# Kernel tuning notes

Measured on AMD Instinct MI355X. Metric: run time of the kernel, lower is better.

Reference implementation:

```python
import jax, jax.numpy as jnp
import numpy as np

EPS = 1e-6

def _sobel_grad_mag(x):
    # x: [B, C, H, W]. Kernels are cross-correlation (as F.conv2d):
    # vertical:   out[i,j] = -x[i-1,j] + x[i+1,j]
    # horizontal: out[i,j] = -x[i,j-1] + x[i,j+1]
    # padding=1 -> zero-pad borders, same spatial output size.
    xp = jnp.pad(x, ((0, 0), (0, 0), (1, 1), (1, 1)))
    gv = xp[:, :, 2:, 1:-1] - xp[:, :, :-2, 1:-1]   # x[i+1,j] - x[i-1,j]
    gh = xp[:, :, 1:-1, 2:] - xp[:, :, 1:-1, :-2]   # x[i,j+1] - x[i,j-1]
    return jnp.sqrt(gv * gv + gh * gh + EPS)

def setup_inputs() -> dict:
    key = jax.random.key(0)
    x = jax.random.normal(key, (8, 64, 256, 256), dtype=jnp.float32)
    return {"x": x}

def reference(x):
    return _sobel_grad_mag(x)
```

## Files before the change

### kernel.cpp

```cpp
#include <hip/hip_runtime.h>
#include <math.h>


#define PLANE_H 256
#define PLANE_W 256
#define VECW 64

__global__ __launch_bounds__(256) void sobel_kernel(const float* __restrict__ x,
                                                    float* __restrict__ out,
                                                    int total_vec) {
    int idx = blockIdx.x * blockDim.x + threadIdx.x;
    if (idx >= total_vec) return;

    int j4    = idx & (VECW - 1);
    int row   = (idx >> 6) & (PLANE_H - 1);
    int plane = idx >> 14;

    size_t base = ((size_t)plane << 16) + ((size_t)row << 8) + ((size_t)j4 << 2);
    const float* p = x + base;

    float4 c  = *(const float4*)p;
    float4 up = (row > 0)           ? *(const float4*)(p - PLANE_W)
                                    : make_float4(0.f, 0.f, 0.f, 0.f);
    float4 dn = (row < PLANE_H - 1) ? *(const float4*)(p + PLANE_W)
                                    : make_float4(0.f, 0.f, 0.f, 0.f);
    float left  = (j4 > 0)        ? p[-1] : 0.f;
    float right = (j4 < VECW - 1) ? p[4]  : 0.f;

    const float eps = 1e-6f;

    float gh0 = c.y   - left;
    float gh1 = c.z   - c.x;
    float gh2 = c.w   - c.y;
    float gh3 = right - c.z;

    float gv0 = dn.x - up.x;
    float gv1 = dn.y - up.y;
    float gv2 = dn.z - up.z;
    float gv3 = dn.w - up.w;

    float4 o;
    o.x = sqrtf(gv0 * gv0 + gh0 * gh0 + eps);
    o.y = sqrtf(gv1 * gv1 + gh1 * gh1 + eps);
    o.z = sqrtf(gv2 * gv2 + gh2 * gh2 + eps);
    o.w = sqrtf(gv3 * gv3 + gh3 * gh3 + eps);

    *(float4*)(out + base) = o;
}

extern "C" void kernel_launch(void* const* d_in, const int* in_sizes, int n_in,
                              void* d_out, int out_size, void* d_ws, size_t ws_size,
                              hipStream_t stream) {
    const float* x = (const float*)d_in[0];
    float* out = (float*)d_out;
    int total_vec = out_size / 4;
    int block = 256;
    int grid = (total_vec + block - 1) / block;
    sobel_kernel<<<grid, block, 0, stream>>>(x, out, total_vec);
}
```

Before: 220.0 us.

## Process four rows per wavefront with register row window and lane shuffles

Each 64-lane wavefront now handles four consecutive rows of a plane. It keeps a sliding window of six float4 rows in registers, so the vertical neighbours are reused instead of reloaded, cutting redundant global reads from about 3x to 1.5x per output row. The left and right neighbour scalars now come from cross-lane shuffles rather than extra unaligned loads. The cost is fewer threads in the grid and a few more registers per thread. The kernel is already memory-bound, so the gain depends on how much the redundant loads were served by cache.

```diff
diff --git a/kernel.cpp b/kernel.cpp
--- a/kernel.cpp
+++ b/kernel.cpp
@@ -4,48 +4,59 @@
 
 #define PLANE_H 256
 #define PLANE_W 256
-#define VECW 64
+#define R 4
 
 __global__ __launch_bounds__(256) void sobel_kernel(const float* __restrict__ x,
-                                                    float* __restrict__ out,
-                                                    int total_vec) {
-    int idx = blockIdx.x * blockDim.x + threadIdx.x;
-    if (idx >= total_vec) return;
+                                                    float* __restrict__ out) {
+    const int tid  = threadIdx.x;
+    const int lane = tid & 63;
+    const int w    = blockIdx.x * 4 + (tid >> 6);
+    const int plane = w >> 6;
+    const int r0    = (w & 63) << 2;
 
-    int j4    = idx & (VECW - 1);
-    int row   = (idx >> 6) & (PLANE_H - 1);
-    int plane = idx >> 14;
-
-    size_t base = ((size_t)plane << 16) + ((size_t)row << 8) + ((size_t)j4 << 2);
+    const size_t base = ((size_t)plane << 16) + ((size_t)r0 << 8) + ((size_t)lane << 2);
     const float* p = x + base;
 
-    float4 c  = *(const float4*)p;
-    float4 up = (row > 0)           ? *(const float4*)(p - PLANE_W)
+    float4 win[R + 2];
+    win[0] = (r0 > 0) ? *(const float4*)(p - PLANE_W) : make_float4(0.f, 0.f, 0.f, 0.f);
+#pragma unroll
+    for (int i = 0; i < R; ++i)
+        win[i + 1] = *(const float4*)(p + (i << 8));
+    win[R + 1] = (r0 + R < PLANE_H) ? *(const float4*)(p + (R << 8))
                                     : make_float4(0.f, 0.f, 0.f, 0.f);
-    float4 dn = (row < PLANE_H - 1) ? *(const float4*)(p + PLANE_W)
-                                    : make_float4(0.f, 0.f, 0.f, 0.f);
-    float left  = (j4 > 0)        ? p[-1] : 0.f;
-    float right = (j4 < VECW - 1) ? p[4]  : 0.f;
 
+    float* po = out + base;
     const float eps = 1e-6f;
 
-    float gh0 = c.y   - left;
-    float gh1 = c.z   - c.x;
-    float gh2 = c.w   - c.y;
-    float gh3 = right - c.z;
+#pragma unroll
+    for (int i = 0; i < R; ++i) {
+        float4 c  = win[i + 1];
+        float4 up = win[i];
+        float4 dn = win[i + 2];
 
-    float gv0 = dn.x - up.x;
-    float gv1 = dn.y - up.y;
-    float gv2 = dn.z - up.z;
-    float gv3 = dn.w - up.w;
+        float left  = __shfl_up(c.w, 1, 64);
+        float right = __shfl_down(c.x, 1, 64);
+        if (lane == 0)  left  = 0.f;
+        if (lane == 63) right = 0.f;
 
-    float4 o;
-    o.x = sqrtf(gv0 * gv0 + gh0 * gh0 + eps);
-    o.y = sqrtf(gv1 * gv1 + gh1 * gh1 + eps);
-    o.z = sqrtf(gv2 * gv2 + gh2 * gh2 + eps);
-    o.w = sqrtf(gv3 * gv3 + gh3 * gh3 + eps);
+        float gh0 = c.y   - left;
+        float gh1 = c.z   - c.x;
+        float gh2 = c.w   - c.y;
+        float gh3 = right - c.z;
 
-    *(float4*)(out + base) = o;
+        float gv0 = dn.x - up.x;
+        float gv1 = dn.y - up.y;
+        float gv2 = dn.z - up.z;
+        float gv3 = dn.w - up.w;
+
+        float4 o;
+        o.x = sqrtf(gv0 * gv0 + gh0 * gh0 + eps);
+        o.y = sqrtf(gv1 * gv1 + gh1 * gh1 + eps);
+        o.z = sqrtf(gv2 * gv2 + gh2 * gh2 + eps);
+        o.w = sqrtf(gv3 * gv3 + gh3 * gh3 + eps);
+
+        *(float4*)(po + (i << 8)) = o;
+    }
 }
 
 extern "C" void kernel_launch(void* const* d_in, const int* in_sizes, int n_in,
@@ -53,8 +64,9 @@
                               hipStream_t stream) {
     const float* x = (const float*)d_in[0];
     float* out = (float*)d_out;
-    int total_vec = out_size / 4;
+    int planes = out_size / (PLANE_H * PLANE_W);
+    int totalWaves = planes * (PLANE_H / R);
     int block = 256;
-    int grid = (total_vec + block - 1) / block;
-    sobel_kernel<<<grid, block, 0, stream>>>(x, out, total_vec);
+    int grid = totalWaves / 4;
+    sobel_kernel<<<grid, block, 0, stream>>>(x, out);
 }
```

Result: slower. 225.5 us (+2.5%).
